# Performance work log

Measured on AMD Instinct MI355X. Metric: run time of the kernel, lower is better.

The kernel has to match this reference:

```python
import jax, jax.numpy as jnp
import numpy as np

B, L, DIN = 16, 4096, 1280
DM, N, R, NL = 128, 16, 8, 2  # d_model=d_inner, d_state, dt_rank, num_layers


def setup_inputs() -> dict:
    key = jax.random.key(0)
    ks = jax.random.split(key, 16)
    f = lambda i, shape, s=0.02: jax.random.normal(ks[i], shape, jnp.float32) * s
    return dict(
        x=jax.random.normal(ks[0], (B, L, DIN), jnp.float32),
        ip_w=f(1, (DM, DIN)), ip_b=f(2, (DM,)),
        in_w=f(3, (NL, 2 * DM, DM)),              # in_proj (no bias), out = [x; z]
        conv_w=f(4, (NL, DM, 2), 0.5), conv_b=f(5, (NL, DM)),  # depthwise causal conv, k=2
        xp_w=f(6, (NL, R + 2 * N, DM)),           # x_proj -> [dt; B; C]
        dt_w=f(7, (NL, DM, R), 0.5), dt_b=f(8, (NL, DM)),
        A_log=jnp.broadcast_to(jnp.log(jnp.arange(1, N + 1, dtype=jnp.float32)), (NL, DM, N)),
        Dp=jnp.ones((NL, DM), jnp.float32),
        out_w=f(9, (NL, DM, DM)),
        ln_g=jnp.ones((DM,), jnp.float32), ln_b=jnp.zeros((DM,), jnp.float32),
        c1_w=f(10, (64, DM)), c1_b=f(11, (64,)),
        c2_w=f(12, (2, 64)), c2_b=f(13, (2,)),
    )


def _mamba(x, in_w, conv_w, conv_b, xp_w, dt_w, dt_b, A_log, Dp, out_w):
    # x: [B,L,DM]
    Bsz, Ls, _ = x.shape
    xz = jnp.einsum('bld,ed->ble', x, in_w)          # [B,L,2*DM]
    u, z = jnp.split(xz, 2, axis=-1)                  # each [B,L,DM]
    # causal depthwise conv, kernel size 2: y_t = w0*u_{t-1} + w1*u_t + b
    u_prev = jnp.pad(u, ((0, 0), (1, 0), (0, 0)))[:, :Ls]
    u = jax.nn.silu(u_prev * conv_w[:, 0] + u * conv_w[:, 1] + conv_b)
    proj = jnp.einsum('bld,ed->ble', u, xp_w)         # [B,L,R+2N]
    dt, Bm, Cm = jnp.split(proj, [R, R + N], axis=-1)
    delta = jax.nn.softplus(jnp.einsum('blr,dr->bld', dt, dt_w) + dt_b)  # [B,L,DM]
    A = -jnp.exp(A_log)                               # [DM,N]

    def step(h, inp):
        d_t, b_t, c_t, u_t = inp                      # [B,DM],[B,N],[B,N],[B,DM]
        dA = jnp.exp(d_t[..., None] * A)              # [B,DM,N]
        h = h * dA + (d_t * u_t)[..., None] * b_t[:, None, :]
        y = jnp.einsum('bdn,bn->bd', h, c_t)
        return h, y

    h0 = jnp.zeros((Bsz, DM, N), x.dtype)
    xs = (delta.transpose(1, 0, 2), Bm.transpose(1, 0, 2),
          Cm.transpose(1, 0, 2), u.transpose(1, 0, 2))
    _, ys = jax.lax.scan(step, h0, xs)                # ys: [L,B,DM]
    y = ys.transpose(1, 0, 2) + u * Dp
    y = y * jax.nn.silu(z)
    return jnp.einsum('bld,ed->ble', y, out_w)


def reference(x, ip_w, ip_b, in_w, conv_w, conv_b, xp_w, dt_w, dt_b, A_log, Dp,
              out_w, ln_g, ln_b, c1_w, c1_b, c2_w, c2_b):
    h = jnp.einsum('bli,di->bld', x, ip_w) + ip_b     # input_proj
    for l in range(NL):                               # residual Mamba blocks
        h = h + _mamba(h, in_w[l], conv_w[l], conv_b[l], xp_w[l], dt_w[l],
                       dt_b[l], A_log[l], Dp[l], out_w[l])
    mu = jnp.mean(h, -1, keepdims=True)
    var = jnp.mean((h - mu) ** 2, -1, keepdims=True)
    h = (h - mu) / jnp.sqrt(var + 1e-5) * ln_g + ln_b # LayerNorm
    p = jnp.mean(h, axis=1)                           # mean pool over seq
    p = jax.nn.relu(p @ c1_w.T + c1_b)                # classifier (dropout=eval/no-op)
    return p @ c2_w.T + c2_b                          # [B,2]
```

## Files before the change

kernel.cpp:

```cpp
#include <hip/hip_runtime.h>
#include <hip/hip_bf16.h>
#include <cstdint>

#define B_   16
#define L_   4096
#define DIN_ 1280
#define DM_  128
#define NS_  16
#define RR_  8
#define NL_  2
#define M_   (B_ * L_)
#define NC_  128
#define CL_  (L_ / NC_)

typedef short short8 __attribute__((ext_vector_type(8)));
typedef float f32x4  __attribute__((ext_vector_type(4)));
typedef unsigned short ushort;
typedef ushort ushort4v __attribute__((ext_vector_type(4)));

__device__ __forceinline__ float silu_f(float x) { return x / (1.f + __expf(-x)); }

__device__ __forceinline__ ushort f2bf(float f) {
  union { float f; uint32_t u; } v; v.f = f;
  uint32_t u = v.u;
  u += 0x7fffu + ((u >> 16) & 1u);
  return (ushort)(u >> 16);
}

__device__ __forceinline__ float bf2f(ushort u) {
  union { uint32_t u; float f; } v; v.u = ((uint32_t)u) << 16; return v.f;
}

__global__ __launch_bounds__(256) void wcvt_k(
    const float* __restrict__ a, int na,
    const float* __restrict__ b, int nb,
    const float* __restrict__ c, int nc,
    ushort* __restrict__ dst, float* __restrict__ poolz)
{
  int i = blockIdx.x * 256 + threadIdx.x;
  const int nw = na + nb + nc;
  if (i < na) dst[i] = f2bf(a[i]);
  else if (i < na + nb) dst[i] = f2bf(b[i - na]);
  else if (i < nw) dst[i] = f2bf(c[i - na - nb]);
  else if (i < nw + B_ * DM_) poolz[i - nw] = 0.f;
}

#define LDK 40
#define LDH 136

__global__ __launch_bounds__(256) void gemm_ipk(
    const float* __restrict__ A, const ushort* __restrict__ W,
    const float* __restrict__ bias, ushort* __restrict__ C)
{
  __shared__ ushort As[128 * LDK];
  __shared__ ushort Ws[128 * LDK];
  const int tid = threadIdx.x;
  const int m0 = blockIdx.y * 128;
  const int K = DIN_;

  const int srow = tid >> 1;
  const int scol = (tid & 1) << 4;
  const float*  gAf = A + (size_t)(m0 + srow) * K + scol;
  const ushort* gW  = W + (size_t)srow * K + scol;

  const int lane = tid & 63;
  const int wv = tid >> 6;
  const int wm = (wv & 1) * 64, wn = (wv >> 1) * 64;
  const int ln15 = lane & 15, quad = lane >> 4;

  f32x4 acc[4][4];
#pragma unroll
  for (int i = 0; i < 4; ++i)
#pragma unroll
    for (int j = 0; j < 4; ++j) acc[i][j] = (f32x4){0.f, 0.f, 0.f, 0.f};

  float4 fa[4];
  short8 w2[2];
#pragma unroll
  for (int j = 0; j < 4; ++j) fa[j] = *(const float4*)(gAf + j * 4);
  w2[0] = *(const short8*)gW;
  w2[1] = *(const short8*)(gW + 8);

  for (int k0 = 0; k0 < K; k0 += 32) {
    __syncthreads();
#pragma unroll
    for (int j = 0; j < 4; ++j) {
      ushort4v a4 = { f2bf(fa[j].x), f2bf(fa[j].y), f2bf(fa[j].z), f2bf(fa[j].w) };
      *(ushort4v*)&As[srow * LDK + scol + j * 4] = a4;
    }
    *(short8*)&Ws[srow * LDK + scol]     = w2[0];
    *(short8*)&Ws[srow * LDK + scol + 8] = w2[1];
    if (k0 + 32 < K) {
#pragma unroll
      for (int j = 0; j < 4; ++j) fa[j] = *(const float4*)(gAf + k0 + 32 + j * 4);
      w2[0] = *(const short8*)(gW + k0 + 32);
      w2[1] = *(const short8*)(gW + k0 + 40);
    }
    __syncthreads();
    short8 aF[4], bF[4];
#pragma unroll
    for (int mt = 0; mt < 4; ++mt)
      aF[mt] = *(const short8*)&As[(wm + mt * 16 + ln15) * LDK + quad * 8];
#pragma unroll
    for (int nt = 0; nt < 4; ++nt)
      bF[nt] = *(const short8*)&Ws[(wn + nt * 16 + ln15) * LDK + quad * 8];
#pragma unroll
    for (int mt = 0; mt < 4; ++mt)
#pragma unroll
      for (int nt = 0; nt < 4; ++nt)
        acc[mt][nt] = __builtin_amdgcn_mfma_f32_16x16x32_bf16(
            aF[mt], bF[nt], acc[mt][nt], 0, 0, 0);
  }

#pragma unroll
  for (int mt = 0; mt < 4; ++mt) {
    const int row = m0 + wm + mt * 16 + quad * 4;
#pragma unroll
    for (int nt = 0; nt < 4; ++nt) {
      const int col = wn + nt * 16 + ln15;
      const float bv = bias[col];
#pragma unroll
      for (int r = 0; r < 4; ++r)
        C[(size_t)(row + r) * DM_ + col] = f2bf(acc[mt][nt][r] + bv);
    }
  }
}

__global__ __launch_bounds__(256) void inx(
    const ushort* __restrict__ A,
    const ushort* __restrict__ W,
    const float* __restrict__ cw, const float* __restrict__ cb,
    const float* __restrict__ xpw,
    const float* __restrict__ dtw,
    const float* __restrict__ dtb,
    ushort* __restrict__ zb, ushort* __restrict__ ub,
    ushort* __restrict__ db, ushort* __restrict__ bcb)
{
  __shared__ ushort As[128 * LDH];
  __shared__ ushort Ws2[128 * LDH];
  __shared__ ushort hprev[128];
  __shared__ float uprev[128];
  const int tid = threadIdx.x;
  const size_t m0 = (size_t)blockIdx.x * 128;
  const int t0 = (int)(m0 & (L_ - 1));

  {
    const int r = tid >> 1, cb2 = (tid & 1) << 6;
    const ushort* gA = A + (size_t)(m0 + r) * DM_ + cb2;
    const ushort* gW = W + (size_t)r * DM_ + cb2;
#pragma unroll
    for (int j = 0; j < 8; ++j) {
      *(short8*)&As[r * LDH + cb2 + j * 8]  = *(const short8*)(gA + j * 8);
      *(short8*)&Ws2[r * LDH + cb2 + j * 8] = *(const short8*)(gW + j * 8);
    }
    if (t0 > 0 && tid < 16)
      *(short8*)&hprev[tid * 8] = *(const short8*)(A + (m0 - 1) * DM_ + tid * 8);
  }
  __syncthreads();

  const int lane = tid & 63;
  const int wv = tid >> 6;
  const int wm = (wv & 1) * 64, wn = (wv >> 1) * 64;
  const int ln15 = lane & 15, quad = lane >> 4;

  f32x4 aU[4][4];
#pragma unroll
  for (int i = 0; i < 4; ++i)
#pragma unroll
    for (int j = 0; j < 4; ++j) aU[i][j] = (f32x4){0.f, 0.f, 0.f, 0.f};
#pragma unroll
  for (int kk = 0; kk < 4; ++kk) {
    short8 aF[4], bF[4];
#pragma unroll
    for (int mt = 0; mt < 4; ++mt)
      aF[mt] = *(const short8*)&As[(wm + mt * 16 + ln15) * LDH + kk * 32 + quad * 8];
#pragma unroll
    for (int nt = 0; nt < 4; ++nt)
      bF[nt] = *(const short8*)&Ws2[(wn + nt * 16 + ln15) * LDH + kk * 32 + quad * 8];
#pragma unroll
    for (int mt = 0; mt < 4; ++mt)
#pragma unroll
      for (int nt = 0; nt < 4; ++nt)
        aU[mt][nt] = __builtin_amdgcn_mfma_f32_16x16x32_bf16(
            aF[mt], bF[nt], aU[mt][nt], 0, 0, 0);
  }
  if (tid < 128) {
    float acc = 0.f;
    if (t0 > 0) {
      const ushort* wr = W + (size_t)tid * DM_;
#pragma unroll
      for (int k0 = 0; k0 < 16; ++k0) {
        short8 wv8 = *(const short8*)(wr + k0 * 8);
        short8 hv8 = *(const short8*)&hprev[k0 * 8];
#pragma unroll
        for (int j = 0; j < 8; ++j)
          acc = fmaf(bf2f((ushort)wv8[j]), bf2f((ushort)hv8[j]), acc);
      }
    }
    uprev[tid] = acc;
  }
  __syncthreads();

  {
    const int r = tid >> 1, cb2 = (tid & 1) << 6;
    const ushort* gW = W + (size_t)(128 + r) * DM_ + cb2;
#pragma unroll
    for (int j = 0; j < 8; ++j)
      *(short8*)&Ws2[r * LDH + cb2 + j * 8] = *(const short8*)(gW + j * 8);
  }
  __syncthreads();

  f32x4 aZ[4][4];
#pragma unroll
  for (int i = 0; i < 4; ++i)
#pragma unroll
    for (int j = 0; j < 4; ++j) aZ[i][j] = (f32x4){0.f, 0.f, 0.f, 0.f};
#pragma unroll
  for (int kk = 0; kk < 4; ++kk) {
    short8 aF[4], bF[4];
#pragma unroll
    for (int mt = 0; mt < 4; ++mt)
      aF[mt] = *(const short8*)&As[(wm + mt * 16 + ln15) * LDH + kk * 32 + quad * 8];
#pragma unroll
    for (int nt = 0; nt < 4; ++nt)
      bF[nt] = *(const short8*)&Ws2[(wn + nt * 16 + ln15) * LDH + kk * 32 + quad * 8];
#pragma unroll
    for (int mt = 0; mt < 4; ++mt)
#pragma unroll
      for (int nt = 0; nt < 4; ++nt)
        aZ[mt][nt] = __builtin_amdgcn_mfma_f32_16x16x32_bf16(
            aF[mt], bF[nt], aZ[mt][nt], 0, 0, 0);
  }
  __syncthreads();

#pragma unroll
  for (int mt = 0; mt < 4; ++mt) {
    const int row = wm + mt * 16 + quad * 4;
#pragma unroll
    for (int nt = 0; nt < 4; ++nt) {
      const int col = wn + nt * 16 + ln15;
#pragma unroll
      for (int r = 0; r < 4; ++r) {
        zb[(m0 + row + r) * DM_ + col] = f2bf(silu_f(aZ[mt][nt][r]));
        As[(row + r) * LDH + col] = f2bf(aU[mt][nt][r]);
      }
    }
  }
  __syncthreads();

  const int dd = tid & 127;
  {
    const float cw0 = cw[dd * 2], cw1 = cw[dd * 2 + 1], cbv = cb[dd];
    const float upv = uprev[dd];
#pragma unroll 4
    for (int i = 0; i < 64; ++i) {
      const int t = i * 2 + (tid >> 7);
      float cur = bf2f(As[t * LDH + dd]);
      float prev = (t == 0) ? upv : bf2f(As[(t - 1) * LDH + dd]);
      float v = silu_f(cw0 * prev + cw1 * cur + cbv);
      ushort vb = f2bf(v);
      Ws2[t * LDH + dd] = vb;
      ub[(m0 + t) * DM_ + dd] = vb;
    }
  }
  __syncthreads();

  float*  pr_s  = (float*)As;
  ushort* bc_s  = As + 2048;
  ushort* xpw_s = As + 6144;
#pragma unroll
  for (int it = 0; it < 24; ++it) {
    int f = it * 256 + tid;
    int e = f >> 7, c = f & 127;
    xpw_s[e * 136 + c] = (e < 40) ? f2bf(xpw[e * 128 + c]) : (ushort)0;
  }
  __syncthreads();

  {
    f32x4 p2[2][3];
#pragma unroll
    for (int i = 0; i < 2; ++i)
#pragma unroll
      for (int j = 0; j < 3; ++j) p2[i][j] = (f32x4){0.f, 0.f, 0.f, 0.f};
#pragma unroll
    for (int kk = 0; kk < 4; ++kk) {
      short8 aF2[2], bF2[3];
#pragma unroll
      for (int m = 0; m < 2; ++m)
        aF2[m] = *(const short8*)&Ws2[(wv * 32 + m * 16 + ln15) * LDH + kk * 32 + quad * 8];
#pragma unroll
      for (int n = 0; n < 3; ++n)
        bF2[n] = *(const short8*)&xpw_s[(n * 16 + ln15) * 136 + kk * 32 + quad * 8];
#pragma unroll
      for (int m = 0; m < 2; ++m)
#pragma unroll
        for (int n = 0; n < 3; ++n)
          p2[m][n] = __builtin_amdgcn_mfma_f32_16x16x32_bf16(
              aF2[m], bF2[n], p2[m][n], 0, 0, 0);
    }
#pragma unroll
    for (int m = 0; m < 2; ++m) {
      const int trow = wv * 32 + m * 16 + quad * 4;
#pragma unroll
      for (int n = 0; n < 3; ++n) {
        const int e = n * 16 + ln15;
#pragma unroll
        for (int r = 0; r < 4; ++r) {
          float v = p2[m][n][r];
          if (e < 8)       pr_s[(trow + r) * 8 + e] = v;
          else if (e < 40) bc_s[(trow + r) * 32 + (e - 8)] = f2bf(v);
        }
      }
    }
  }
  __syncthreads();

  {
    const float dtbv = dtb[dd];
    const float4 w0 = *(const float4*)(dtw + dd * 8);
    const float4 w1 = *(const float4*)(dtw + dd * 8 + 4);
#pragma unroll 4
    for (int i = 0; i < 64; ++i) {
      const int t = i * 2 + (tid >> 7);
      const float4 p0 = *(const float4*)(pr_s + t * 8);
      const float4 p1 = *(const float4*)(pr_s + t * 8 + 4);
      float a = dtbv;
      a = fmaf(p0.x, w0.x, a); a = fmaf(p0.y, w0.y, a);
      a = fmaf(p0.z, w0.z, a); a = fmaf(p0.w, w0.w, a);
      a = fmaf(p1.x, w1.x, a); a = fmaf(p1.y, w1.y, a);
      a = fmaf(p1.z, w1.z, a); a = fmaf(p1.w, w1.w, a);
      float sp = (a > 20.f) ? a : log1pf(__expf(a));
      db[(m0 + t) * DM_ + dd] = f2bf(sp);
    }
#pragma unroll
    for (int i = 0; i < 16; ++i) {
      int f = i * 256 + tid;
      int t = f >> 5, e = f & 31;
      bcb[(m0 + t) * 32 + e] = bc_s[t * 32 + e];
    }
  }
}

__global__ __launch_bounds__(128) void scan_h(
    const ushort* __restrict__ delta, const ushort* __restrict__ u,
    const ushort* __restrict__ BC,
    float* __restrict__ hend, float* __restrict__ Ssum)
{
  const int d = threadIdx.x;
  const int chunk = blockIdx.x, b = blockIdx.y;
  float h[NS_];
#pragma unroll
  for (int n = 0; n < NS_; ++n) h[n] = 0.f;
  float S = 0.f;
  const size_t rowbase = (size_t)b * L_ + (size_t)chunk * CL_;
  float dlt = bf2f(delta[rowbase * DM_ + d]);
  float uu  = bf2f(u[rowbase * DM_ + d]);
  for (int s = 0; s < CL_; ++s) {
    const uint32_t* Br = (const uint32_t*)(BC + (rowbase + s) * 32);
    float Bv[NS_];
#pragma unroll
    for (int q = 0; q < 8; ++q) {
      uint32_t w = Br[q];
      Bv[2 * q]     = __uint_as_float(w << 16);
      Bv[2 * q + 1] = __uint_as_float(w & 0xffff0000u);
    }
    float dn = 0.f, un = 0.f;
    if (s + 1 < CL_) {
      dn = bf2f(delta[(rowbase + s + 1) * DM_ + d]);
      un = bf2f(u[(rowbase + s + 1) * DM_ + d]);
    }
    const float du = dlt * uu;
    S += dlt;
    const float E = __expf(-dlt);
    float dA = 1.f;
#pragma unroll
    for (int n = 0; n < NS_; ++n) {
      dA *= E;
      h[n] = fmaf(h[n], dA, du * Bv[n]);
    }
    dlt = dn; uu = un;
  }
  const size_t o = ((size_t)b * NC_ + chunk) * DM_ + d;
  float4* hp = (float4*)(hend + o * NS_);
#pragma unroll
  for (int q = 0; q < 4; ++q)
    hp[q] = make_float4(h[q * 4], h[q * 4 + 1], h[q * 4 + 2], h[q * 4 + 3]);
  Ssum[o] = S;
}

__global__ __launch_bounds__(256) void scan_comb(
    const float* __restrict__ hend, const float* __restrict__ Ssum,
    float* __restrict__ hstart)
{
  const int idx = blockIdx.x * 256 + threadIdx.x;
  const int n = idx & 15;
  const int d = (idx >> 4) & 127;
  const int b = idx >> 11;
  const float na = -(float)(n + 1);
  const size_t base = (size_t)b * NC_;
  float hs = 0.f;
  float he[4], Sv[4];
#pragma unroll
  for (int j = 0; j < 4; ++j) {
    const size_t o = (base + j) * DM_ + d;
    he[j] = hend[o * NS_ + n];
    Sv[j] = Ssum[o];
  }
  for (int c0 = 0; c0 < NC_; c0 += 4) {
    float E[4], hc[4];
#pragma unroll
    for (int j = 0; j < 4; ++j) { E[j] = __expf(na * Sv[j]); hc[j] = he[j]; }
    if (c0 + 4 < NC_) {
#pragma unroll
      for (int j = 0; j < 4; ++j) {
        const size_t o = (base + c0 + 4 + j) * DM_ + d;
        he[j] = hend[o * NS_ + n];
        Sv[j] = Ssum[o];
      }
    }
#pragma unroll
    for (int j = 0; j < 4; ++j) {
      const size_t o = (base + c0 + j) * DM_ + d;
      hstart[o * NS_ + n] = hs;
      hs = fmaf(E[j], hs, hc[j]);
    }
  }
}

template<int LAST>
__global__ __launch_bounds__(256) void syop(
    const ushort* __restrict__ delta, const ushort* __restrict__ u,
    const ushort* __restrict__ zbuf, const ushort* __restrict__ BC,
    const float* __restrict__ Dpv, const float* __restrict__ hstart,
    const ushort* __restrict__ W,
    ushort* __restrict__ hb, float* __restrict__ pool)
{
  __shared__ ushort sm[2 * 128 * LDH];
  __shared__ float ps[4][128];
  ushort* y_lds = sm;
  ushort* Ws = sm + 128 * LDH;
  const int tid = threadIdx.x;
  const size_t m0 = (size_t)blockIdx.x * 128;
  const int b = (int)(m0 >> 12);
  const int c0 = (int)((m0 & (L_ - 1)) >> 5);

  {
    const int r = tid >> 1, cb2 = (tid & 1) << 6;
    const ushort* gW = W + (size_t)r * DM_ + cb2;
#pragma unroll
    for (int j = 0; j < 8; ++j)
      *(short8*)&Ws[r * LDH + cb2 + j * 8] = *(const short8*)(gW + j * 8);
  }

  const int d = tid & 127;
  const float Dd = Dpv[d];
#pragma unroll
  for (int rep = 0; rep < 2; ++rep) {
    const int cl = rep * 2 + (tid >> 7);
    const size_t rowbase = m0 + (size_t)cl * CL_;
    float h[NS_];
    const size_t o = ((size_t)b * NC_ + (c0 + cl)) * DM_ + d;
    const float4* hp = (const float4*)(hstart + o * NS_);
#pragma unroll
    for (int q = 0; q < 4; ++q) {
      float4 v = hp[q];
      h[q * 4] = v.x; h[q * 4 + 1] = v.y; h[q * 4 + 2] = v.z; h[q * 4 + 3] = v.w;
    }
    float dlt = bf2f(delta[rowbase * DM_ + d]);
    float uu  = bf2f(u[rowbase * DM_ + d]);
    float zz  = bf2f(zbuf[rowbase * DM_ + d]);
    for (int s = 0; s < CL_; ++s) {
      const uint32_t* Br = (const uint32_t*)(BC + (rowbase + s) * 32);
      float Bv[NS_], Cv[NS_];
#pragma unroll
      for (int q = 0; q < 8; ++q) {
        uint32_t wB = Br[q], wC = Br[8 + q];
        Bv[2 * q]     = __uint_as_float(wB << 16);
        Bv[2 * q + 1] = __uint_as_float(wB & 0xffff0000u);
        Cv[2 * q]     = __uint_as_float(wC << 16);
        Cv[2 * q + 1] = __uint_as_float(wC & 0xffff0000u);
      }
      float dn = 0.f, un = 0.f, zn = 0.f;
      if (s + 1 < CL_) {
        dn = bf2f(delta[(rowbase + s + 1) * DM_ + d]);
        un = bf2f(u[(rowbase + s + 1) * DM_ + d]);
        zn = bf2f(zbuf[(rowbase + s + 1) * DM_ + d]);
      }
      const float du = dlt * uu;
      float yv = uu * Dd;
      const float E = __expf(-dlt);
      float dA = 1.f;
#pragma unroll
      for (int n = 0; n < NS_; ++n) {
        dA *= E;
        h[n] = fmaf(h[n], dA, du * Bv[n]);
        yv = fmaf(h[n], Cv[n], yv);
      }
      y_lds[(cl * 32 + s) * LDH + d] = f2bf(yv * zz);
      dlt = dn; uu = un; zz = zn;
    }
  }
  __syncthreads();

  const int lane = tid & 63;
  const int wv = tid >> 6;
  const int wm = (wv & 1) * 64, wn = (wv >> 1) * 64;
  const int ln15 = lane & 15, quad = lane >> 4;
  f32x4 acc[4][4];
#pragma unroll
  for (int i = 0; i < 4; ++i)
#pragma unroll
    for (int j = 0; j < 4; ++j) acc[i][j] = (f32x4){0.f, 0.f, 0.f, 0.f};
#pragma unroll
  for (int kk = 0; kk < 4; ++kk) {
    short8 aF[4], bF[4];
#pragma unroll
    for (int mt = 0; mt < 4; ++mt)
      aF[mt] = *(const short8*)&y_lds[(wm + mt * 16 + ln15) * LDH + kk * 32 + quad * 8];
#pragma unroll
    for (int nt = 0; nt < 4; ++nt)
      bF[nt] = *(const short8*)&Ws[(wn + nt * 16 + ln15) * LDH + kk * 32 + quad * 8];
#pragma unroll
    for (int mt = 0; mt < 4; ++mt)
#pragma unroll
      for (int nt = 0; nt < 4; ++nt)
        acc[mt][nt] = __builtin_amdgcn_mfma_f32_16x16x32_bf16(
            aF[mt], bF[nt], acc[mt][nt], 0, 0, 0);
  }

  if constexpr (LAST == 0) {
#pragma unroll
    for (int mt = 0; mt < 4; ++mt) {
      const int row = wm + mt * 16 + quad * 4;
#pragma unroll
      for (int nt = 0; nt < 4; ++nt) {
        const int col = wn + nt * 16 + ln15;
#pragma unroll
        for (int r = 0; r < 4; ++r) {
          size_t off = (m0 + row + r) * DM_ + col;
          hb[off] = f2bf(acc[mt][nt][r] + bf2f(hb[off]));
        }
      }
    }
  } else {
    float* hT = (float*)sm;
    __syncthreads();
#pragma unroll
    for (int mt = 0; mt < 4; ++mt) {
      const int lrow = wm + mt * 16 + quad * 4;
#pragma unroll
      for (int nt = 0; nt < 4; ++nt) {
        const int col = wn + nt * 16 + ln15;
#pragma unroll
        for (int r = 0; r < 4; ++r) {
          size_t off = (m0 + lrow + r) * DM_ + col;
          hT[(lrow + r) * 132 + col] = acc[mt][nt][r] + bf2f(hb[off]);
        }
      }
    }
    __syncthreads();
    float a0 = 0.f, a1 = 0.f;
    for (int i = 0; i < 32; ++i) {
      const int row = wv * 32 + i;
      float x0 = hT[row * 132 + lane], x1 = hT[row * 132 + lane + 64];
      float s = x0 + x1, sq = x0 * x0 + x1 * x1;
      for (int off = 32; off; off >>= 1) { s += __shfl_xor(s, off); sq += __shfl_xor(sq, off); }
      float mu = s * (1.f / 128.f);
      float var = sq * (1.f / 128.f) - mu * mu;
      float rstd = rsqrtf(var + 1e-5f);
      a0 += (x0 - mu) * rstd;
      a1 += (x1 - mu) * rstd;
    }
    ps[wv][lane] = a0;
    ps[wv][lane + 64] = a1;
    __syncthreads();
    if (tid < 128)
      atomicAdd(&pool[b * DM_ + tid],
                ps[0][tid] + ps[1][tid] + ps[2][tid] + ps[3][tid]);
  }
}

__global__ __launch_bounds__(256) void headk(
    const float* __restrict__ pool,
    const float* __restrict__ lng, const float* __restrict__ lnb,
    const float* __restrict__ c1w, const float* __restrict__ c1b,
    const float* __restrict__ c2w, const float* __restrict__ c2b,
    float* __restrict__ out)
{
  __shared__ float pool_s[16][128];
  __shared__ float p1[16][64];
  const int tid = threadIdx.x;
  for (int i = tid; i < 16 * 128; i += 256) {
    int dd = i & 127;
    pool_s[i >> 7][dd] = pool[i] * (1.f / (float)L_) * lng[dd] + lnb[dd];
  }
  __syncthreads();
  for (int i = tid; i < 16 * 64; i += 256) {
    int b = i >> 6, j = i & 63;
    float acc = c1b[j];
    for (int dd = 0; dd < 128; ++dd) acc += pool_s[b][dd] * c1w[j * 128 + dd];
    p1[b][j] = fmaxf(acc, 0.f);
  }
  __syncthreads();
  if (tid < 32) {
    int b = tid >> 1, k = tid & 1;
    float acc = c2b[k];
    for (int j = 0; j < 64; ++j) acc += p1[b][j] * c2w[k * 64 + j];
    out[b * 2 + k] = acc;
  }
}

extern "C" void kernel_launch(void* const* d_in, const int* in_sizes, int n_in,
                              void* d_out, int out_size, void* d_ws, size_t ws_size,
                              hipStream_t stream)
{
  (void)in_sizes; (void)n_in; (void)out_size; (void)ws_size;
  const float* x    = (const float*)d_in[0];
  const float* ipw  = (const float*)d_in[1];
  const float* ipb  = (const float*)d_in[2];
  const float* inw  = (const float*)d_in[3];
  const float* cw   = (const float*)d_in[4];
  const float* cb   = (const float*)d_in[5];
  const float* xpw  = (const float*)d_in[6];
  const float* dtw  = (const float*)d_in[7];
  const float* dtb  = (const float*)d_in[8];
  const float* Dpv  = (const float*)d_in[10];
  const float* outw = (const float*)d_in[11];
  const float* lng  = (const float*)d_in[12];
  const float* lnb  = (const float*)d_in[13];
  const float* c1w  = (const float*)d_in[14];
  const float* c1b  = (const float*)d_in[15];
  const float* c2w  = (const float*)d_in[16];
  const float* c2b  = (const float*)d_in[17];

  const size_t SZ  = (size_t)M_ * DM_;
  const size_t HSZ = (size_t)B_ * NC_ * DM_ * NS_;

  ushort* us   = (ushort*)d_ws;
  ushort* hb   = us;
  ushort* zb   = hb + SZ;
  ushort* ub   = zb + SZ;
  ushort* db   = ub + SZ;
  ushort* bcb  = db + SZ;
  ushort* wb   = bcb + (size_t)M_ * 32;
  const int NIP = DM_ * DIN_;
  const int NIN = NL_ * 2 * DM_ * DM_;
  const int NOW = NL_ * DM_ * DM_;
  ushort* wip  = wb;
  ushort* win  = wb + NIP;
  ushort* wout = win + NIN;

  float* fs     = (float*)(wb + (NIP + NIN + NOW));
  float* hend   = fs;
  float* hstart = hend + HSZ;
  float* Ssum   = hstart + HSZ;
  float* pool   = Ssum + (size_t)B_ * NC_ * DM_;

  const int NW = NIP + NIN + NOW;
  wcvt_k<<<(NW + B_ * DM_ + 255) / 256, 256, 0, stream>>>(
      ipw, NIP, inw, NIN, outw, NOW, wb, pool);

  gemm_ipk<<<dim3(1, M_ / 128), 256, 0, stream>>>(x, wip, ipb, hb);

  for (int l = 0; l < NL_; ++l) {
    inx<<<M_ / 128, 256, 0, stream>>>(
        hb, win + (size_t)l * 2 * DM_ * DM_,
        cw + l * DM_ * 2, cb + l * DM_,
        xpw + l * 40 * DM_, dtw + l * DM_ * RR_, dtb + l * DM_,
        zb, ub, db, bcb);
    scan_h<<<dim3(NC_, B_), 128, 0, stream>>>(db, ub, bcb, hend, Ssum);
    scan_comb<<<(B_ * DM_ * NS_) / 256, 256, 0, stream>>>(hend, Ssum, hstart);
    if (l + 1 < NL_) {
      syop<0><<<M_ / 128, 256, 0, stream>>>(
          db, ub, zb, bcb, Dpv + l * DM_, hstart,
          wout + (size_t)l * DM_ * DM_, hb, nullptr);
    } else {
      syop<1><<<M_ / 128, 256, 0, stream>>>(
          db, ub, zb, bcb, Dpv + l * DM_, hstart,
          wout + (size_t)l * DM_ * DM_, hb, pool);
    }
  }

  headk<<<1, 256, 0, stream>>>(pool, lng, lnb, c1w, c1b, c2w, c2b, (float*)d_out);
}
```

Measured before the change: 818.2 us.

## Double syop threads per tile, break dA power chain, use stable softplus

The syop kernel now launches 512 threads, so each thread scans one 32-step chunk instead of two in sequence. The output MFMA tile is split across 8 waves, and the LayerNorm/pool reduction is adjusted to match. In scan_h and syop, the serial 16-step dA *= E chain becomes a tree of power products, which shortens the dependency chain at the cost of a few extra multiplies. Softplus switches to a branch-free max+log1p(exp(-|a|)) form using fast intrinsics, which may change rounding slightly.

```diff
diff --git a/kernel.cpp b/kernel.cpp
--- a/kernel.cpp
+++ b/kernel.cpp
@@ -30,6 +30,18 @@
 __device__ __forceinline__ float bf2f(ushort u) {
   union { uint32_t u; float f; } v; v.u = ((uint32_t)u) << 16; return v.f;
 }
+
+#define POW16(E1, dAv)                                            \
+  const float E2 = (E1) * (E1);                                   \
+  const float E3 = E2 * (E1);                                     \
+  const float E4 = E2 * E2;                                       \
+  const float E5 = E4 * (E1);                                     \
+  const float E6 = E4 * E2;                                       \
+  const float E7 = E4 * E3;                                       \
+  const float E8 = E4 * E4;                                       \
+  const float dAv[16] = { (E1), E2, E3, E4, E5, E6, E7, E8,       \
+                          E8 * (E1), E8 * E2, E8 * E3, E8 * E4,   \
+                          E8 * E5, E8 * E6, E8 * E7, E8 * E8 };
 
 __global__ __launch_bounds__(256) void wcvt_k(
     const float* __restrict__ a, int na,
@@ -329,7 +341,7 @@
       a = fmaf(p0.z, w0.z, a); a = fmaf(p0.w, w0.w, a);
       a = fmaf(p1.x, w1.x, a); a = fmaf(p1.y, w1.y, a);
       a = fmaf(p1.z, w1.z, a); a = fmaf(p1.w, w1.w, a);
-      float sp = (a > 20.f) ? a : log1pf(__expf(a));
+      float sp = fmaxf(a, 0.f) + __logf(1.f + __expf(-fabsf(a)));
       db[(m0 + t) * DM_ + dd] = f2bf(sp);
     }
 #pragma unroll
@@ -371,13 +383,11 @@
     }
     const float du = dlt * uu;
     S += dlt;
-    const float E = __expf(-dlt);
-    float dA = 1.f;
-#pragma unroll
-    for (int n = 0; n < NS_; ++n) {
-      dA *= E;
-      h[n] = fmaf(h[n], dA, du * Bv[n]);
-    }
+    const float E1 = __expf(-dlt);
+    POW16(E1, dAv)
+#pragma unroll
+    for (int n = 0; n < NS_; ++n)
+      h[n] = fmaf(h[n], dAv[n], du * Bv[n]);
     dlt = dn; uu = un;
   }
   const size_t o = ((size_t)b * NC_ + chunk) * DM_ + d;
@@ -428,7 +438,7 @@
 }
 
 template<int LAST>
-__global__ __launch_bounds__(256) void syop(
+__global__ __launch_bounds__(512) void syop(
     const ushort* __restrict__ delta, const ushort* __restrict__ u,
     const ushort* __restrict__ zbuf, const ushort* __restrict__ BC,
     const float* __restrict__ Dpv, const float* __restrict__ hstart,
@@ -436,7 +446,7 @@
     ushort* __restrict__ hb, float* __restrict__ pool)
 {
   __shared__ ushort sm[2 * 128 * LDH];
-  __shared__ float ps[4][128];
+  __shared__ float ps[8][128];
   ushort* y_lds = sm;
   ushort* Ws = sm + 128 * LDH;
   const int tid = threadIdx.x;
@@ -445,18 +455,17 @@
   const int c0 = (int)((m0 & (L_ - 1)) >> 5);
 
   {
-    const int r = tid >> 1, cb2 = (tid & 1) << 6;
-    const ushort* gW = W + (size_t)r * DM_ + cb2;
-#pragma unroll
-    for (int j = 0; j < 8; ++j)
-      *(short8*)&Ws[r * LDH + cb2 + j * 8] = *(const short8*)(gW + j * 8);
+    const int r = tid >> 2, cc = (tid & 3) << 5;
+    const ushort* gW = W + (size_t)r * DM_ + cc;
+#pragma unroll
+    for (int j = 0; j < 4; ++j)
+      *(short8*)&Ws[r * LDH + cc + j * 8] = *(const short8*)(gW + j * 8);
   }
 
   const int d = tid & 127;
+  const int cl = tid >> 7;
   const float Dd = Dpv[d];
-#pragma unroll
-  for (int rep = 0; rep < 2; ++rep) {
-    const int cl = rep * 2 + (tid >> 7);
+  {
     const size_t rowbase = m0 + (size_t)cl * CL_;
     float h[NS_];
     const size_t o = ((size_t)b * NC_ + (c0 + cl)) * DM_ + d;
@@ -488,12 +497,11 @@
       }
       const float du = dlt * uu;
       float yv = uu * Dd;
-      const float E = __expf(-dlt);
-      float dA = 1.f;
+      const float E1 = __expf(-dlt);
+      POW16(E1, dAv)
 #pragma unroll
       for (int n = 0; n < NS_; ++n) {
-        dA *= E;
-        h[n] = fmaf(h[n], dA, du * Bv[n]);
+        h[n] = fmaf(h[n], dAv[n], du * Bv[n]);
         yv = fmaf(h[n], Cv[n], yv);
       }
       y_lds[(cl * 32 + s) * LDH + d] = f2bf(yv * zz);
@@ -504,24 +512,24 @@
 
   const int lane = tid & 63;
   const int wv = tid >> 6;
-  const int wm = (wv & 1) * 64, wn = (wv >> 1) * 64;
+  const int wm = (wv >> 1) * 32, wn = (wv & 1) * 64;
   const int ln15 = lane & 15, quad = lane >> 4;
-  f32x4 acc[4][4];
-#pragma unroll
-  for (int i = 0; i < 4; ++i)
+  f32x4 acc[2][4];
+#pragma unroll
+  for (int i = 0; i < 2; ++i)
 #pragma unroll
     for (int j = 0; j < 4; ++j) acc[i][j] = (f32x4){0.f, 0.f, 0.f, 0.f};
 #pragma unroll
   for (int kk = 0; kk < 4; ++kk) {
-    short8 aF[4], bF[4];
-#pragma unroll
-    for (int mt = 0; mt < 4; ++mt)
+    short8 aF[2], bF[4];
+#pragma unroll
+    for (int mt = 0; mt < 2; ++mt)
       aF[mt] = *(const short8*)&y_lds[(wm + mt * 16 + ln15) * LDH + kk * 32 + quad * 8];
 #pragma unroll
     for (int nt = 0; nt < 4; ++nt)
       bF[nt] = *(const short8*)&Ws[(wn + nt * 16 + ln15) * LDH + kk * 32 + quad * 8];
 #pragma unroll
-    for (int mt = 0; mt < 4; ++mt)
+    for (int mt = 0; mt < 2; ++mt)
 #pragma unroll
       for (int nt = 0; nt < 4; ++nt)
         acc[mt][nt] = __builtin_amdgcn_mfma_f32_16x16x32_bf16(
@@ -530,7 +538,7 @@
 
   if constexpr (LAST == 0) {
 #pragma unroll
-    for (int mt = 0; mt < 4; ++mt) {
+    for (int mt = 0; mt < 2; ++mt) {
       const int row = wm + mt * 16 + quad * 4;
 #pragma unroll
       for (int nt = 0; nt < 4; ++nt) {
@@ -546,7 +554,7 @@
     float* hT = (float*)sm;
     __syncthreads();
 #pragma unroll
-    for (int mt = 0; mt < 4; ++mt) {
+    for (int mt = 0; mt < 2; ++mt) {
       const int lrow = wm + mt * 16 + quad * 4;
 #pragma unroll
       for (int nt = 0; nt < 4; ++nt) {
@@ -560,8 +568,8 @@
     }
     __syncthreads();
     float a0 = 0.f, a1 = 0.f;
-    for (int i = 0; i < 32; ++i) {
-      const int row = wv * 32 + i;
+    for (int i = 0; i < 16; ++i) {
+      const int row = wv * 16 + i;
       float x0 = hT[row * 132 + lane], x1 = hT[row * 132 + lane + 64];
       float s = x0 + x1, sq = x0 * x0 + x1 * x1;
       for (int off = 32; off; off >>= 1) { s += __shfl_xor(s, off); sq += __shfl_xor(sq, off); }
@@ -574,9 +582,12 @@
     ps[wv][lane] = a0;
     ps[wv][lane + 64] = a1;
     __syncthreads();
-    if (tid < 128)
-      atomicAdd(&pool[b * DM_ + tid],
-                ps[0][tid] + ps[1][tid] + ps[2][tid] + ps[3][tid]);
+    if (tid < 128) {
+      float s = 0.f;
+#pragma unroll
+      for (int w = 0; w < 8; ++w) s += ps[w][tid];
+      atomicAdd(&pool[b * DM_ + tid], s);
+    }
   }
 }
 
@@ -671,11 +682,11 @@
     scan_h<<<dim3(NC_, B_), 128, 0, stream>>>(db, ub, bcb, hend, Ssum);
     scan_comb<<<(B_ * DM_ * NS_) / 256, 256, 0, stream>>>(hend, Ssum, hstart);
     if (l + 1 < NL_) {
-      syop<0><<<M_ / 128, 256, 0, stream>>>(
+      syop<0><<<M_ / 128, 512, 0, stream>>>(
           db, ub, zb, bcb, Dpv + l * DM_, hstart,
           wout + (size_t)l * DM_ * DM_, hb, nullptr);
     } else {
-      syop<1><<<M_ / 128, 256, 0, stream>>>(
+      syop<1><<<M_ / 128, 512, 0, stream>>>(
           db, ub, zb, bcb, Dpv + l * DM_, hstart,
           wout + (size_t)l * DM_ * DM_, hb, pool);
     }
```

After: 742.2 us. -9.3%, faster.
